# Optimization experiments

Measured on AMD Instinct MI355X. Metric: run time of the kernel, lower is better.

The kernel has to match this reference:

```python
import jax, jax.numpy as jnp
import numpy as np

N_NODES = 10000
N_EDGES = 640000
NF = 128      # n_features
NH = 128      # n_hidden
NT = 128      # n_targets
LN_EPS = 1e-5


def _layer_norm(h, gamma, beta):
    mu = jnp.mean(h, axis=-1, keepdims=True)
    var = jnp.var(h, axis=-1, keepdims=True)
    return (h - mu) * jax.lax.rsqrt(var + LN_EPS) * gamma + beta


def _mlp(h, W1, b1, gamma, beta, W2, b2):
    h = jax.nn.relu(h @ W1 + b1)
    h = _layer_norm(h, gamma, beta)
    return h @ W2 + b2


def setup_inputs() -> dict:
    key = jax.random.key(0)
    ks = jax.random.split(key, 12)
    s_in = 1.0 / np.sqrt(NF + NH)
    s_h = 1.0 / np.sqrt(NH)
    return {
        "x": jax.random.normal(ks[0], (N_NODES, NF), dtype=jnp.float32),
        "edge_idx": jax.random.randint(ks[1], (2, N_EDGES), 0, N_NODES, dtype=jnp.int32),
        "edge_attr": jax.random.normal(ks[2], (N_EDGES, NH), dtype=jnp.float32),
        # node_mlp_1 params
        "W1a": jax.random.normal(ks[3], (NF + NH, NH), dtype=jnp.float32) * s_in,
        "b1a": jnp.zeros((NH,), dtype=jnp.float32),
        "g1": jnp.ones((NH,), dtype=jnp.float32),
        "be1": jnp.zeros((NH,), dtype=jnp.float32),
        "W1b": jax.random.normal(ks[4], (NH, NH), dtype=jnp.float32) * s_h,
        "b1b": jnp.zeros((NH,), dtype=jnp.float32),
        # node_mlp_2 params
        "W2a": jax.random.normal(ks[5], (NF + NH, NH), dtype=jnp.float32) * s_in,
        "b2a": jnp.zeros((NH,), dtype=jnp.float32),
        "g2": jnp.ones((NH,), dtype=jnp.float32),
        "be2": jnp.zeros((NH,), dtype=jnp.float32),
        "W2b": jax.random.normal(ks[6], (NH, NT), dtype=jnp.float32) * s_h,
        "b2b": jnp.zeros((NT,), dtype=jnp.float32),
    }


def reference(x, edge_idx, edge_attr, W1a, b1a, g1, be1, W1b, b1b,
              W2a, b2a, g2, be2, W2b, b2b):
    row, col = edge_idx[0], edge_idx[1]
    # gather source-node features and run per-edge MLP
    h = jnp.concatenate([x[col], edge_attr], axis=1)        # [E, NF+NH]
    h = _mlp(h, W1a, b1a, g1, be1, W1b, b1b)                 # [E, NH]
    # scatter_mean into target nodes
    sums = jax.ops.segment_sum(h, row, num_segments=N_NODES)
    cnt = jax.ops.segment_sum(jnp.ones((h.shape[0],), h.dtype), row,
                              num_segments=N_NODES)
    agg = sums / jnp.maximum(cnt, 1.0)[:, None]              # [N, NH]
    out = jnp.concatenate([x, agg], axis=1)                  # [N, NF+NH]
    return _mlp(out, W2a, b2a, g2, be2, W2b, b2b)            # [N, NT]
```

## Files before the change

### kernel.cpp

```cpp
#include <hip/hip_runtime.h>
#include <hip/hip_bf16.h>

#define NN 10000
#define NE 640000
#define NF 128
#define NH 128
#define NT 128
#define KA 256
#define LN_EPS 1e-5f

typedef __bf16 bf16x8 __attribute__((ext_vector_type(8)));
typedef float floatx4 __attribute__((ext_vector_type(4)));
typedef float nfloat4 __attribute__((ext_vector_type(4)));

__device__ inline unsigned short f2bf(float f) {
    unsigned int u = __float_as_uint(f);
    u += 0x7FFFu + ((u >> 16) & 1u);
    return (unsigned short)(u >> 16);
}

__device__ inline bf16x8 load_frag(const unsigned short* p) {
    uint4 u = *(const uint4*)p;
    return __builtin_bit_cast(bf16x8, u);
}

__global__ __launch_bounds__(256) void conv_weights(
    const float* __restrict__ W1a, const float* __restrict__ W1b,
    const float* __restrict__ W2a, const float* __restrict__ W2b,
    unsigned short* __restrict__ wp1a, unsigned short* __restrict__ wp1b,
    unsigned short* __restrict__ wp2a, unsigned short* __restrict__ wp2b)
{
    int tid = blockIdx.x * 256 + threadIdx.x;
    const float* src;
    unsigned short* dst;
    int t, nks;
    if (tid < 4096)        { src = W1a; dst = wp1a; t = tid;         nks = 8; }
    else if (tid < 6144)   { src = W1b; dst = wp1b; t = tid - 4096;  nks = 4; }
    else if (tid < 10240)  { src = W2a; dst = wp2a; t = tid - 6144;  nks = 8; }
    else if (tid < 12288)  { src = W2b; dst = wp2b; t = tid - 10240; nks = 4; }
    else return;

    const int f = t >> 6, l = t & 63;
    const int ct = f / nks, ks = f - ct * nks;
    const int n  = ct * 16 + (l & 15);
    const int k0 = ks * 32 + (l >> 4) * 8;
    unsigned short tmp[8];
#pragma unroll
    for (int j = 0; j < 8; ++j)
        tmp[j] = f2bf(src[(k0 + j) * 128 + n]);
    *(uint4*)&dst[t * 8] = *(const uint4*)tmp;
}

__global__ __launch_bounds__(256) void hist_kernel(
    const int* __restrict__ row, int* __restrict__ hist)
{
    int e = blockIdx.x * 256 + threadIdx.x;
    if (e < NE) atomicAdd(&hist[row[e]], 1);
}

__global__ __launch_bounds__(256) void scan_kernel(
    const int* __restrict__ hist, int* __restrict__ row_start,
    int* __restrict__ cursor)
{
    __shared__ int partials[256];
    const int t = threadIdx.x;
    const int base = t * 40;
    int s = 0;
    for (int i = 0; i < 40; ++i) {
        int b = base + i;
        if (b < NN) s += hist[b];
    }
    partials[t] = s;
    __syncthreads();
    int pre = 0;
    for (int i = 0; i < t; ++i) pre += partials[i];
    int run = pre;
    for (int i = 0; i < 40; ++i) {
        int b = base + i;
        if (b < NN) {
            row_start[b] = run;
            cursor[b] = run;
            run += hist[b];
        }
    }
    if (t == 255) row_start[NN] = NE;
}

__global__ __launch_bounds__(256) void scatter_kernel(
    const int* __restrict__ row, int* __restrict__ cursor,
    int* __restrict__ perm)
{
    int e = blockIdx.x * 256 + threadIdx.x;
    if (e < NE) {
        int p = atomicAdd(&cursor[row[e]], 1);
        perm[p] = e;
    }
}

__global__ __launch_bounds__(256) void edge_mlp_kernel(
    const float* __restrict__ x,
    const int* __restrict__ erow, const int* __restrict__ ecol,
    const float* __restrict__ eattr,
    const int* __restrict__ perm,
    const unsigned short* __restrict__ wp1a, const float* __restrict__ b1a,
    const float* __restrict__ g1, const float* __restrict__ be1,
    const unsigned short* __restrict__ wp1b,
    float* __restrict__ sums)
{
    __shared__ float accbuf[64][132];
    __shared__ unsigned short Ttile[4][16][NH + 8];
    __shared__ int rows_s[64];
    unsigned short (*Atile)[16][KA + 8] = (unsigned short (*)[16][KA + 8])accbuf;

    const int wave = threadIdx.x >> 6;
    const int lane = threadIdx.x & 63;
    const int e0 = blockIdx.x * 64 + wave * 16;

    if (threadIdx.x < 64) {
        int e = perm[blockIdx.x * 64 + threadIdx.x];
        rows_s[threadIdx.x] = erow[e];
    }

    {
        const int lrow = lane >> 2;
        const int lq   = lane & 3;
        const int e = perm[e0 + lrow];
        const int src = ecol[e];
        const nfloat4* xr = (const nfloat4*)(x + src * NF);
        const nfloat4* ar = (const nfloat4*)(eattr + (size_t)e * NH);
        unsigned short* Ar = &Atile[wave][lrow][0];
#pragma unroll
        for (int it = 0; it < 8; ++it) {
            int c4 = lq + it * 4;
            nfloat4 v = xr[c4];
            uint2 w;
            w.x = (unsigned)f2bf(v.x) | ((unsigned)f2bf(v.y) << 16);
            w.y = (unsigned)f2bf(v.z) | ((unsigned)f2bf(v.w) << 16);
            *(uint2*)&Ar[c4 * 4] = w;
            nfloat4 v2 = __builtin_nontemporal_load(ar + c4);
            uint2 w2;
            w2.x = (unsigned)f2bf(v2.x) | ((unsigned)f2bf(v2.y) << 16);
            w2.y = (unsigned)f2bf(v2.z) | ((unsigned)f2bf(v2.w) << 16);
            *(uint2*)&Ar[128 + c4 * 4] = w2;
        }
    }
    __syncthreads();

    const int lm  = lane & 15;
    const int lq4 = lane >> 4;

    bf16x8 a1[8];
#pragma unroll
    for (int ks = 0; ks < 8; ++ks)
        a1[ks] = load_frag(&Atile[wave][lm][ks * 32 + lq4 * 8]);

    floatx4 acc1[8];
#pragma unroll
    for (int ct = 0; ct < 8; ++ct) {
        floatx4 acc = {0.f, 0.f, 0.f, 0.f};
        const unsigned short* wr = wp1a + (ct * 8 * 64 + lane) * 8;
#pragma unroll
        for (int ks = 0; ks < 8; ++ks) {
            bf16x8 b = load_frag(wr + ks * 512);
            acc = __builtin_amdgcn_mfma_f32_16x16x32_bf16(a1[ks], b, acc, 0, 0, 0);
        }
        acc1[ct] = acc;
    }

    float sum_[4] = {0, 0, 0, 0}, sq_[4] = {0, 0, 0, 0};
#pragma unroll
    for (int ct = 0; ct < 8; ++ct) {
        const float bb = b1a[ct * 16 + lm];
#pragma unroll
        for (int i = 0; i < 4; ++i) {
            float v = acc1[ct][i] + bb;
            v = fmaxf(v, 0.f);
            acc1[ct][i] = v;
            sum_[i] += v;
            sq_[i]  += v * v;
        }
    }
#pragma unroll
    for (int m = 1; m < 16; m <<= 1) {
#pragma unroll
        for (int i = 0; i < 4; ++i) {
            sum_[i] += __shfl_xor(sum_[i], m, 64);
            sq_[i]  += __shfl_xor(sq_[i],  m, 64);
        }
    }
    float mu[4], rs[4];
#pragma unroll
    for (int i = 0; i < 4; ++i) {
        mu[i] = sum_[i] * (1.f / NH);
        float var = sq_[i] * (1.f / NH) - mu[i] * mu[i];
        rs[i] = rsqrtf(var + LN_EPS);
    }
#pragma unroll
    for (int ct = 0; ct < 8; ++ct) {
        const int c = ct * 16 + lm;
        const float gg = g1[c], bb = be1[c];
#pragma unroll
        for (int i = 0; i < 4; ++i) {
            float nv = (acc1[ct][i] - mu[i]) * rs[i] * gg + bb;
            Ttile[wave][lq4 * 4 + i][c] = f2bf(nv);
        }
    }
    __syncthreads();

    bf16x8 a2[4];
#pragma unroll
    for (int ks = 0; ks < 4; ++ks)
        a2[ks] = load_frag(&Ttile[wave][lm][ks * 32 + lq4 * 8]);

#pragma unroll
    for (int ct = 0; ct < 8; ++ct) {
        floatx4 acc = {0.f, 0.f, 0.f, 0.f};
        const unsigned short* wr = wp1b + (ct * 4 * 64 + lane) * 8;
#pragma unroll
        for (int ks = 0; ks < 4; ++ks) {
            bf16x8 b = load_frag(wr + ks * 512);
            acc = __builtin_amdgcn_mfma_f32_16x16x32_bf16(a2[ks], b, acc, 0, 0, 0);
        }
        const int c = ct * 16 + lm;
#pragma unroll
        for (int i = 0; i < 4; ++i)
            accbuf[wave * 16 + lq4 * 4 + i][c] = acc[i];
    }
    __syncthreads();

    {
        const int t = threadIdx.x;
        const int c = t & 127;
        const int jb = (t >> 7) * 32;
        float a = 0.f;
        int cur = rows_s[jb];
#pragma unroll 4
        for (int j = jb; j < jb + 32; ++j) {
            a += accbuf[j][c];
            int nxt = (j + 1 < jb + 32) ? rows_s[j + 1] : -1;
            if (nxt != cur) {
                atomicAdd(&sums[cur * NH + c], a);
                a = 0.f;
                cur = nxt;
            }
        }
    }
}

__global__ __launch_bounds__(256) void node_mlp_kernel(
    const float* __restrict__ x,
    const float* __restrict__ sums, const int* __restrict__ row_start,
    const float* __restrict__ b1b,
    const unsigned short* __restrict__ wp2a, const float* __restrict__ b2a,
    const float* __restrict__ g2, const float* __restrict__ be2,
    const unsigned short* __restrict__ wp2b, const float* __restrict__ b2b,
    float* __restrict__ out)
{
    __shared__ unsigned short Atile[4][16][KA + 8];
    __shared__ unsigned short Ttile[4][16][NH + 8];

    const int wave = threadIdx.x >> 6;
    const int lane = threadIdx.x & 63;
    const int n0 = blockIdx.x * 64 + wave * 16;

    {
        const int lrow = lane >> 2;
        const int lq   = lane & 3;
        int n = n0 + lrow;
        if (n >= NN) n = NN - 1;
        const int cntn = row_start[n + 1] - row_start[n];
        const float inv  = (cntn > 0) ? (1.f / (float)cntn) : 1.f;
        const float addb = (cntn > 0) ? 1.f : 0.f;
        const float4* xr = (const float4*)(x + n * NF);
        const float4* sr = (const float4*)(sums + n * NH);
        const float4* br = (const float4*)b1b;
        unsigned short* Ar = &Atile[wave][lrow][0];
#pragma unroll
        for (int it = 0; it < 8; ++it) {
            int c4 = lq + it * 4;
            float4 v = xr[c4];
            uint2 w;
            w.x = (unsigned)f2bf(v.x) | ((unsigned)f2bf(v.y) << 16);
            w.y = (unsigned)f2bf(v.z) | ((unsigned)f2bf(v.w) << 16);
            *(uint2*)&Ar[c4 * 4] = w;
            float4 v2 = sr[c4];
            float4 bv = br[c4];
            float a0 = v2.x * inv + addb * bv.x;
            float a1 = v2.y * inv + addb * bv.y;
            float a2 = v2.z * inv + addb * bv.z;
            float a3 = v2.w * inv + addb * bv.w;
            uint2 w2;
            w2.x = (unsigned)f2bf(a0) | ((unsigned)f2bf(a1) << 16);
            w2.y = (unsigned)f2bf(a2) | ((unsigned)f2bf(a3) << 16);
            *(uint2*)&Ar[128 + c4 * 4] = w2;
        }
    }
    __syncthreads();

    const int lm  = lane & 15;
    const int lq4 = lane >> 4;

    bf16x8 a1[8];
#pragma unroll
    for (int ks = 0; ks < 8; ++ks)
        a1[ks] = load_frag(&Atile[wave][lm][ks * 32 + lq4 * 8]);

    floatx4 acc1[8];
#pragma unroll
    for (int ct = 0; ct < 8; ++ct) {
        floatx4 acc = {0.f, 0.f, 0.f, 0.f};
        const unsigned short* wr = wp2a + (ct * 8 * 64 + lane) * 8;
#pragma unroll
        for (int ks = 0; ks < 8; ++ks) {
            bf16x8 b = load_frag(wr + ks * 512);
            acc = __builtin_amdgcn_mfma_f32_16x16x32_bf16(a1[ks], b, acc, 0, 0, 0);
        }
        acc1[ct] = acc;
    }

    float sum_[4] = {0, 0, 0, 0}, sq_[4] = {0, 0, 0, 0};
#pragma unroll
    for (int ct = 0; ct < 8; ++ct) {
        const float bb = b2a[ct * 16 + lm];
#pragma unroll
        for (int i = 0; i < 4; ++i) {
            float v = acc1[ct][i] + bb;
            v = fmaxf(v, 0.f);
            acc1[ct][i] = v;
            sum_[i] += v;
            sq_[i]  += v * v;
        }
    }
#pragma unroll
    for (int m = 1; m < 16; m <<= 1) {
#pragma unroll
        for (int i = 0; i < 4; ++i) {
            sum_[i] += __shfl_xor(sum_[i], m, 64);
            sq_[i]  += __shfl_xor(sq_[i],  m, 64);
        }
    }
    float mu[4], rs[4];
#pragma unroll
    for (int i = 0; i < 4; ++i) {
        mu[i] = sum_[i] * (1.f / NH);
        float var = sq_[i] * (1.f / NH) - mu[i] * mu[i];
        rs[i] = rsqrtf(var + LN_EPS);
    }
#pragma unroll
    for (int ct = 0; ct < 8; ++ct) {
        const int c = ct * 16 + lm;
        const float gg = g2[c], bb = be2[c];
#pragma unroll
        for (int i = 0; i < 4; ++i) {
            float nv = (acc1[ct][i] - mu[i]) * rs[i] * gg + bb;
            Ttile[wave][lq4 * 4 + i][c] = f2bf(nv);
        }
    }
    __syncthreads();

    bf16x8 a2[4];
#pragma unroll
    for (int ks = 0; ks < 4; ++ks)
        a2[ks] = load_frag(&Ttile[wave][lm][ks * 32 + lq4 * 8]);

#pragma unroll
    for (int ct = 0; ct < 8; ++ct) {
        floatx4 acc = {0.f, 0.f, 0.f, 0.f};
        const unsigned short* wr = wp2b + (ct * 4 * 64 + lane) * 8;
#pragma unroll
        for (int ks = 0; ks < 4; ++ks) {
            bf16x8 b = load_frag(wr + ks * 512);
            acc = __builtin_amdgcn_mfma_f32_16x16x32_bf16(a2[ks], b, acc, 0, 0, 0);
        }
        const int c = ct * 16 + lm;
        const float bb = b2b[c];
#pragma unroll
        for (int i = 0; i < 4; ++i) {
            int n = n0 + lq4 * 4 + i;
            if (n < NN) out[n * NT + c] = acc[i] + bb;
        }
    }
}

extern "C" void kernel_launch(void* const* d_in, const int* in_sizes, int n_in,
                              void* d_out, int out_size, void* d_ws, size_t ws_size,
                              hipStream_t stream) {
    const float* x     = (const float*)d_in[0];
    const int*   eidx  = (const int*)d_in[1];
    const float* eattr = (const float*)d_in[2];
    const float* W1a = (const float*)d_in[3];
    const float* b1a = (const float*)d_in[4];
    const float* g1  = (const float*)d_in[5];
    const float* be1 = (const float*)d_in[6];
    const float* W1b = (const float*)d_in[7];
    const float* b1b = (const float*)d_in[8];
    const float* W2a = (const float*)d_in[9];
    const float* b2a = (const float*)d_in[10];
    const float* g2  = (const float*)d_in[11];
    const float* be2 = (const float*)d_in[12];
    const float* W2b = (const float*)d_in[13];
    const float* b2b = (const float*)d_in[14];

    char* ws = (char*)d_ws;
    float* sums     = (float*)ws;
    int*   hist     = (int*)(ws + 5120000);
    int*   cursor   = (int*)(ws + 5160000);
    int*   row_start= (int*)(ws + 5200000);
    int*   perm     = (int*)(ws + 5240064);
    unsigned short* wp1a = (unsigned short*)(ws + 7800064);
    unsigned short* wp1b = (unsigned short*)(ws + 7865600);
    unsigned short* wp2a = (unsigned short*)(ws + 7898368);
    unsigned short* wp2b = (unsigned short*)(ws + 7963904);

    const int* erow = eidx;
    const int* ecol = eidx + NE;

    (void)hipMemsetAsync(ws, 0, 5160000, stream);
    conv_weights<<<48, 256, 0, stream>>>(W1a, W1b, W2a, W2b, wp1a, wp1b, wp2a, wp2b);
    hist_kernel<<<(NE + 255) / 256, 256, 0, stream>>>(erow, hist);
    scan_kernel<<<1, 256, 0, stream>>>(hist, row_start, cursor);
    scatter_kernel<<<(NE + 255) / 256, 256, 0, stream>>>(erow, cursor, perm);
    edge_mlp_kernel<<<NE / 64, 256, 0, stream>>>(x, erow, ecol, eattr, perm,
                                                 wp1a, b1a, g1, be1, wp1b, sums);
    node_mlp_kernel<<<(NN + 63) / 64, 256, 0, stream>>>(x, sums, row_start, b1b,
                                                        wp2a, b2a, g2, be2, wp2b, b2b,
                                                        (float*)d_out);
}
```

Measured before the change: 716.7 us.

## Split edge MLP output columns across waves, keeping weight fragments in registers

The edge MLP kernel is restructured so each wave owns two 16-column output tiles for all 64 edges of the block, instead of all 128 columns for its own 16 edges. Each wave now loads its weight fragments once into registers, where before every wave streamed the full weight matrices from global memory. The A operand is staged in LDS in fragment-major order, and the LayerNorm statistics are combined across waves through a small shared partials buffer. The accumulation buffer uses a rotated (swizzled) layout to avoid bank conflicts, and a launch-bounds occupancy hint is added. In exchange it needs more block-wide syncs and a cross-wave LayerNorm reduction.

Result: no change. 709.8 us (-1.0%).

```diff
diff --git a/kernel.cpp b/kernel.cpp
--- a/kernel.cpp
+++ b/kernel.cpp
@@ -97,7 +97,7 @@
     }
 }
 
-__global__ __launch_bounds__(256) void edge_mlp_kernel(
+__global__ __launch_bounds__(256, 3) void edge_mlp_kernel(
     const float* __restrict__ x,
     const int* __restrict__ erow, const int* __restrict__ ecol,
     const float* __restrict__ eattr,
@@ -107,139 +107,182 @@
     const unsigned short* __restrict__ wp1b,
     float* __restrict__ sums)
 {
-    __shared__ float accbuf[64][132];
-    __shared__ unsigned short Ttile[4][16][NH + 8];
+    __shared__ __align__(16) unsigned short Afrag[16384];
+    __shared__ unsigned short Ttile[64][NH + 8];
+    __shared__ float2 partials[4][64];
+    __shared__ float2 murs[64];
     __shared__ int rows_s[64];
-    unsigned short (*Atile)[16][KA + 8] = (unsigned short (*)[16][KA + 8])accbuf;
 
     const int wave = threadIdx.x >> 6;
     const int lane = threadIdx.x & 63;
-    const int e0 = blockIdx.x * 64 + wave * 16;
+    const int lm   = lane & 15;
+    const int lq4  = lane >> 4;
+    const int e0   = blockIdx.x * 64;
+
+    if (threadIdx.x < 64)
+        rows_s[threadIdx.x] = erow[perm[e0 + threadIdx.x]];
+
+    {
+        const int r = wave * 16 + lm;
+        const int e = perm[e0 + r];
+        const int scol = ecol[e];
+        const nfloat4* xr = (const nfloat4*)(x + (size_t)scol * NF) + lq4 * 2;
+        const nfloat4* ar = (const nfloat4*)(eattr + (size_t)e * NH) + lq4 * 2;
+        unsigned short* dst = &Afrag[(wave * 8) * 512 + lane * 8];
+#pragma unroll
+        for (int ks = 0; ks < 8; ++ks) {
+            nfloat4 v0, v1;
+            if (ks < 4) {
+                v0 = xr[ks * 8];
+                v1 = xr[ks * 8 + 1];
+            } else {
+                v0 = __builtin_nontemporal_load(ar + (ks - 4) * 8);
+                v1 = __builtin_nontemporal_load(ar + (ks - 4) * 8 + 1);
+            }
+            uint4 wv;
+            wv.x = (unsigned)f2bf(v0.x) | ((unsigned)f2bf(v0.y) << 16);
+            wv.y = (unsigned)f2bf(v0.z) | ((unsigned)f2bf(v0.w) << 16);
+            wv.z = (unsigned)f2bf(v1.x) | ((unsigned)f2bf(v1.y) << 16);
+            wv.w = (unsigned)f2bf(v1.z) | ((unsigned)f2bf(v1.w) << 16);
+            *(uint4*)(dst + ks * 512) = wv;
+        }
+    }
+
+    bf16x8 b1f[2][8];
+#pragma unroll
+    for (int c = 0; c < 2; ++c) {
+        const int ct = wave * 2 + c;
+#pragma unroll
+        for (int ks = 0; ks < 8; ++ks)
+            b1f[c][ks] = load_frag(&wp1a[((ct * 8 + ks) * 64 + lane) * 8]);
+    }
+
+    __syncthreads();
+
+    floatx4 acc1[4][2];
+#pragma unroll
+    for (int mt = 0; mt < 4; ++mt) {
+        bf16x8 a[8];
+#pragma unroll
+        for (int ks = 0; ks < 8; ++ks)
+            a[ks] = load_frag(&Afrag[(mt * 8 + ks) * 512 + lane * 8]);
+#pragma unroll
+        for (int c = 0; c < 2; ++c) {
+            floatx4 acc = {0.f, 0.f, 0.f, 0.f};
+#pragma unroll
+            for (int ks = 0; ks < 8; ++ks)
+                acc = __builtin_amdgcn_mfma_f32_16x16x32_bf16(a[ks], b1f[c][ks], acc, 0, 0, 0);
+            acc1[mt][c] = acc;
+        }
+    }
+
+    const float bb0 = b1a[(wave * 2 + 0) * 16 + lm];
+    const float bb1 = b1a[(wave * 2 + 1) * 16 + lm];
+#pragma unroll
+    for (int mt = 0; mt < 4; ++mt) {
+#pragma unroll
+        for (int i = 0; i < 4; ++i) {
+            float v0 = fmaxf(acc1[mt][0][i] + bb0, 0.f);
+            float v1 = fmaxf(acc1[mt][1][i] + bb1, 0.f);
+            acc1[mt][0][i] = v0;
+            acc1[mt][1][i] = v1;
+            float s = v0 + v1;
+            float q = v0 * v0 + v1 * v1;
+#pragma unroll
+            for (int m = 1; m < 16; m <<= 1) {
+                s += __shfl_xor(s, m, 64);
+                q += __shfl_xor(q, m, 64);
+            }
+            if (lm == 0)
+                partials[wave][mt * 16 + lq4 * 4 + i] = make_float2(s, q);
+        }
+    }
+    __syncthreads();
 
     if (threadIdx.x < 64) {
-        int e = perm[blockIdx.x * 64 + threadIdx.x];
-        rows_s[threadIdx.x] = erow[e];
-    }
-
-    {
-        const int lrow = lane >> 2;
-        const int lq   = lane & 3;
-        const int e = perm[e0 + lrow];
-        const int src = ecol[e];
-        const nfloat4* xr = (const nfloat4*)(x + src * NF);
-        const nfloat4* ar = (const nfloat4*)(eattr + (size_t)e * NH);
-        unsigned short* Ar = &Atile[wave][lrow][0];
-#pragma unroll
-        for (int it = 0; it < 8; ++it) {
-            int c4 = lq + it * 4;
-            nfloat4 v = xr[c4];
-            uint2 w;
-            w.x = (unsigned)f2bf(v.x) | ((unsigned)f2bf(v.y) << 16);
-            w.y = (unsigned)f2bf(v.z) | ((unsigned)f2bf(v.w) << 16);
-            *(uint2*)&Ar[c4 * 4] = w;
-            nfloat4 v2 = __builtin_nontemporal_load(ar + c4);
-            uint2 w2;
-            w2.x = (unsigned)f2bf(v2.x) | ((unsigned)f2bf(v2.y) << 16);
-            w2.y = (unsigned)f2bf(v2.z) | ((unsigned)f2bf(v2.w) << 16);
-            *(uint2*)&Ar[128 + c4 * 4] = w2;
-        }
-    }
-    __syncthreads();
-
-    const int lm  = lane & 15;
-    const int lq4 = lane >> 4;
-
-    bf16x8 a1[8];
-#pragma unroll
-    for (int ks = 0; ks < 8; ++ks)
-        a1[ks] = load_frag(&Atile[wave][lm][ks * 32 + lq4 * 8]);
-
-    floatx4 acc1[8];
-#pragma unroll
-    for (int ct = 0; ct < 8; ++ct) {
-        floatx4 acc = {0.f, 0.f, 0.f, 0.f};
-        const unsigned short* wr = wp1a + (ct * 8 * 64 + lane) * 8;
-#pragma unroll
-        for (int ks = 0; ks < 8; ++ks) {
-            bf16x8 b = load_frag(wr + ks * 512);
-            acc = __builtin_amdgcn_mfma_f32_16x16x32_bf16(a1[ks], b, acc, 0, 0, 0);
-        }
-        acc1[ct] = acc;
-    }
-
-    float sum_[4] = {0, 0, 0, 0}, sq_[4] = {0, 0, 0, 0};
-#pragma unroll
-    for (int ct = 0; ct < 8; ++ct) {
-        const float bb = b1a[ct * 16 + lm];
-#pragma unroll
-        for (int i = 0; i < 4; ++i) {
-            float v = acc1[ct][i] + bb;
-            v = fmaxf(v, 0.f);
-            acc1[ct][i] = v;
-            sum_[i] += v;
-            sq_[i]  += v * v;
-        }
-    }
-#pragma unroll
-    for (int m = 1; m < 16; m <<= 1) {
-#pragma unroll
-        for (int i = 0; i < 4; ++i) {
-            sum_[i] += __shfl_xor(sum_[i], m, 64);
-            sq_[i]  += __shfl_xor(sq_[i],  m, 64);
-        }
-    }
-    float mu[4], rs[4];
-#pragma unroll
-    for (int i = 0; i < 4; ++i) {
-        mu[i] = sum_[i] * (1.f / NH);
-        float var = sq_[i] * (1.f / NH) - mu[i] * mu[i];
-        rs[i] = rsqrtf(var + LN_EPS);
-    }
-#pragma unroll
-    for (int ct = 0; ct < 8; ++ct) {
-        const int c = ct * 16 + lm;
-        const float gg = g1[c], bb = be1[c];
-#pragma unroll
-        for (int i = 0; i < 4; ++i) {
-            float nv = (acc1[ct][i] - mu[i]) * rs[i] * gg + bb;
-            Ttile[wave][lq4 * 4 + i][c] = f2bf(nv);
-        }
-    }
-    __syncthreads();
-
-    bf16x8 a2[4];
-#pragma unroll
-    for (int ks = 0; ks < 4; ++ks)
-        a2[ks] = load_frag(&Ttile[wave][lm][ks * 32 + lq4 * 8]);
-
-#pragma unroll
-    for (int ct = 0; ct < 8; ++ct) {
-        floatx4 acc = {0.f, 0.f, 0.f, 0.f};
-        const unsigned short* wr = wp1b + (ct * 4 * 64 + lane) * 8;
-#pragma unroll
-        for (int ks = 0; ks < 4; ++ks) {
-            bf16x8 b = load_frag(wr + ks * 512);
-            acc = __builtin_amdgcn_mfma_f32_16x16x32_bf16(a2[ks], b, acc, 0, 0, 0);
-        }
-        const int c = ct * 16 + lm;
-#pragma unroll
-        for (int i = 0; i < 4; ++i)
-            accbuf[wave * 16 + lq4 * 4 + i][c] = acc[i];
+        float s = 0.f, q = 0.f;
+#pragma unroll
+        for (int w2 = 0; w2 < 4; ++w2) {
+            float2 p = partials[w2][threadIdx.x];
+            s += p.x; q += p.y;
+        }
+        float mu = s * (1.f / NH);
+        float var = q * (1.f / NH) - mu * mu;
+        murs[threadIdx.x] = make_float2(mu, rsqrtf(var + LN_EPS));
+    }
+    __syncthreads();
+
+    bf16x8 b2f[2][4];
+#pragma unroll
+    for (int c = 0; c < 2; ++c) {
+        const int ct = wave * 2 + c;
+#pragma unroll
+        for (int ks = 0; ks < 4; ++ks)
+            b2f[c][ks] = load_frag(&wp1b[((ct * 4 + ks) * 64 + lane) * 8]);
+    }
+
+    const float gg0 = g1[(wave * 2 + 0) * 16 + lm];
+    const float ee0 = be1[(wave * 2 + 0) * 16 + lm];
+    const float gg1 = g1[(wave * 2 + 1) * 16 + lm];
+    const float ee1 = be1[(wave * 2 + 1) * 16 + lm];
+#pragma unroll
+    for (int mt = 0; mt < 4; ++mt) {
+#pragma unroll
+        for (int i = 0; i < 4; ++i) {
+            const int row = mt * 16 + lq4 * 4 + i;
+            float2 mr = murs[row];
+            float n0 = (acc1[mt][0][i] - mr.x) * mr.y * gg0 + ee0;
+            float n1 = (acc1[mt][1][i] - mr.x) * mr.y * gg1 + ee1;
+            Ttile[row][(wave * 2 + 0) * 16 + lm] = f2bf(n0);
+            Ttile[row][(wave * 2 + 1) * 16 + lm] = f2bf(n1);
+        }
+    }
+    __syncthreads();
+
+    floatx4 acc2[4][2];
+#pragma unroll
+    for (int mt = 0; mt < 4; ++mt) {
+        bf16x8 a[4];
+#pragma unroll
+        for (int ks = 0; ks < 4; ++ks)
+            a[ks] = load_frag(&Ttile[mt * 16 + lm][ks * 32 + lq4 * 8]);
+#pragma unroll
+        for (int c = 0; c < 2; ++c) {
+            floatx4 acc = {0.f, 0.f, 0.f, 0.f};
+#pragma unroll
+            for (int ks = 0; ks < 4; ++ks)
+                acc = __builtin_amdgcn_mfma_f32_16x16x32_bf16(a[ks], b2f[c][ks], acc, 0, 0, 0);
+            acc2[mt][c] = acc;
+        }
+    }
+
+    float* accbuf = (float*)Afrag;
+#pragma unroll
+    for (int mt = 0; mt < 4; ++mt) {
+#pragma unroll
+        for (int c = 0; c < 2; ++c) {
+            const int col = (wave * 2 + c) * 16 + lm;
+#pragma unroll
+            for (int i = 0; i < 4; ++i) {
+                const int row = mt * 16 + lq4 * 4 + i;
+                accbuf[row * 128 + ((col + row * 4) & 127)] = acc2[mt][c][i];
+            }
+        }
     }
     __syncthreads();
 
     {
         const int t = threadIdx.x;
-        const int c = t & 127;
+        const int cc = t & 127;
         const int jb = (t >> 7) * 32;
         float a = 0.f;
         int cur = rows_s[jb];
 #pragma unroll 4
         for (int j = jb; j < jb + 32; ++j) {
-            a += accbuf[j][c];
+            a += accbuf[j * 128 + ((cc + j * 4) & 127)];
             int nxt = (j + 1 < jb + 32) ? rows_s[j + 1] : -1;
             if (nxt != cur) {
-                atomicAdd(&sums[cur * NH + c], a);
+                atomicAdd(&sums[cur * NH + cc], a);
                 a = 0.f;
                 cur = nxt;
             }
```

## Load edge MLP A-fragments directly from global and slim shared memory

Applied to the files above, without the earlier changes.

The edge MLP kernel now loads each lane's x and edge_attr slices straight into the MFMA A-fragment registers, converting them with native bf16 casts. This removes the shared-memory staging tile and its block barrier. The LayerNorm output tile is aliased into each wave's private slice of the accumulation buffer, with only a compiler memory fence instead of __syncthreads. The accumulation buffer is unpadded and column-swizzled to avoid bank conflicts, and launch bounds request 4 blocks per CU. The per-lane global loads are less coalesced than the old cooperative row loads, and forcing occupancy could increase register pressure.

After: 773.9 us. +8.0%, slower.

```diff
diff --git a/kernel.cpp b/kernel.cpp
--- a/kernel.cpp
+++ b/kernel.cpp
@@ -22,6 +22,13 @@
 __device__ inline bf16x8 load_frag(const unsigned short* p) {
     uint4 u = *(const uint4*)p;
     return __builtin_bit_cast(bf16x8, u);
+}
+
+__device__ inline bf16x8 cvt8(nfloat4 v0, nfloat4 v1) {
+    bf16x8 r;
+    r[0] = (__bf16)v0.x; r[1] = (__bf16)v0.y; r[2] = (__bf16)v0.z; r[3] = (__bf16)v0.w;
+    r[4] = (__bf16)v1.x; r[5] = (__bf16)v1.y; r[6] = (__bf16)v1.z; r[7] = (__bf16)v1.w;
+    return r;
 }
 
 __global__ __launch_bounds__(256) void conv_weights(
@@ -97,7 +104,7 @@
     }
 }
 
-__global__ __launch_bounds__(256) void edge_mlp_kernel(
+__global__ __launch_bounds__(256, 4) void edge_mlp_kernel(
     const float* __restrict__ x,
     const int* __restrict__ erow, const int* __restrict__ ecol,
     const float* __restrict__ eattr,
@@ -107,52 +114,36 @@
     const unsigned short* __restrict__ wp1b,
     float* __restrict__ sums)
 {
-    __shared__ float accbuf[64][132];
-    __shared__ unsigned short Ttile[4][16][NH + 8];
+    __shared__ __align__(16) float accbuf[64 * 128];
     __shared__ int rows_s[64];
-    unsigned short (*Atile)[16][KA + 8] = (unsigned short (*)[16][KA + 8])accbuf;
 
     const int wave = threadIdx.x >> 6;
     const int lane = threadIdx.x & 63;
-    const int e0 = blockIdx.x * 64 + wave * 16;
-
-    if (threadIdx.x < 64) {
-        int e = perm[blockIdx.x * 64 + threadIdx.x];
-        rows_s[threadIdx.x] = erow[e];
-    }
-
-    {
-        const int lrow = lane >> 2;
-        const int lq   = lane & 3;
-        const int e = perm[e0 + lrow];
-        const int src = ecol[e];
-        const nfloat4* xr = (const nfloat4*)(x + src * NF);
-        const nfloat4* ar = (const nfloat4*)(eattr + (size_t)e * NH);
-        unsigned short* Ar = &Atile[wave][lrow][0];
-#pragma unroll
-        for (int it = 0; it < 8; ++it) {
-            int c4 = lq + it * 4;
-            nfloat4 v = xr[c4];
-            uint2 w;
-            w.x = (unsigned)f2bf(v.x) | ((unsigned)f2bf(v.y) << 16);
-            w.y = (unsigned)f2bf(v.z) | ((unsigned)f2bf(v.w) << 16);
-            *(uint2*)&Ar[c4 * 4] = w;
-            nfloat4 v2 = __builtin_nontemporal_load(ar + c4);
-            uint2 w2;
-            w2.x = (unsigned)f2bf(v2.x) | ((unsigned)f2bf(v2.y) << 16);
-            w2.y = (unsigned)f2bf(v2.z) | ((unsigned)f2bf(v2.w) << 16);
-            *(uint2*)&Ar[128 + c4 * 4] = w2;
-        }
-    }
-    __syncthreads();
-
-    const int lm  = lane & 15;
-    const int lq4 = lane >> 4;
+    const int lm   = lane & 15;
+    const int lq4  = lane >> 4;
+    const int e0   = blockIdx.x * 64;
+
+    if (threadIdx.x < 64)
+        rows_s[threadIdx.x] = erow[perm[e0 + threadIdx.x]];
+
+    const int e    = perm[e0 + wave * 16 + lm];
+    const int scol = ecol[e];
+    const nfloat4* xr = (const nfloat4*)(x + (size_t)scol * NF) + lq4 * 2;
+    const nfloat4* ar = (const nfloat4*)(eattr + (size_t)e * NH) + lq4 * 2;
 
     bf16x8 a1[8];
 #pragma unroll
-    for (int ks = 0; ks < 8; ++ks)
-        a1[ks] = load_frag(&Atile[wave][lm][ks * 32 + lq4 * 8]);
+    for (int ks = 0; ks < 4; ++ks) {
+        nfloat4 v0 = xr[ks * 8];
+        nfloat4 v1 = xr[ks * 8 + 1];
+        a1[ks] = cvt8(v0, v1);
+    }
+#pragma unroll
+    for (int ks = 0; ks < 4; ++ks) {
+        nfloat4 v0 = __builtin_nontemporal_load(ar + ks * 8);
+        nfloat4 v1 = __builtin_nontemporal_load(ar + ks * 8 + 1);
+        a1[4 + ks] = cvt8(v0, v1);
+    }
 
     floatx4 acc1[8];
 #pragma unroll
@@ -195,6 +186,8 @@
         float var = sq_[i] * (1.f / NH) - mu[i] * mu[i];
         rs[i] = rsqrtf(var + LN_EPS);
     }
+
+    unsigned short* Tw = (unsigned short*)(accbuf + wave * 16 * 128);
 #pragma unroll
     for (int ct = 0; ct < 8; ++ct) {
         const int c = ct * 16 + lm;
@@ -202,15 +195,15 @@
 #pragma unroll
         for (int i = 0; i < 4; ++i) {
             float nv = (acc1[ct][i] - mu[i]) * rs[i] * gg + bb;
-            Ttile[wave][lq4 * 4 + i][c] = f2bf(nv);
-        }
-    }
-    __syncthreads();
+            Tw[(lq4 * 4 + i) * 136 + c] = __builtin_bit_cast(unsigned short, (__bf16)nv);
+        }
+    }
+    asm volatile("" ::: "memory");
 
     bf16x8 a2[4];
 #pragma unroll
     for (int ks = 0; ks < 4; ++ks)
-        a2[ks] = load_frag(&Ttile[wave][lm][ks * 32 + lq4 * 8]);
+        a2[ks] = load_frag(&Tw[lm * 136 + ks * 32 + lq4 * 8]);
 
 #pragma unroll
     for (int ct = 0; ct < 8; ++ct) {
@@ -223,23 +216,25 @@
         }
         const int c = ct * 16 + lm;
 #pragma unroll
-        for (int i = 0; i < 4; ++i)
-            accbuf[wave * 16 + lq4 * 4 + i][c] = acc[i];
+        for (int i = 0; i < 4; ++i) {
+            const int r = wave * 16 + lq4 * 4 + i;
+            accbuf[r * 128 + ((c + r * 4) & 127)] = acc[i];
+        }
     }
     __syncthreads();
 
     {
         const int t = threadIdx.x;
-        const int c = t & 127;
+        const int cc = t & 127;
         const int jb = (t >> 7) * 32;
         float a = 0.f;
         int cur = rows_s[jb];
 #pragma unroll 4
         for (int j = jb; j < jb + 32; ++j) {
-            a += accbuf[j][c];
+            a += accbuf[j * 128 + ((cc + j * 4) & 127)];
             int nxt = (j + 1 < jb + 32) ? rows_s[j + 1] : -1;
             if (nxt != cur) {
-                atomicAdd(&sums[cur * NH + c], a);
+                atomicAdd(&sums[cur * NH + cc], a);
                 a = 0.f;
                 cur = nxt;
             }
```

## Fuse whole GNN pipeline into one persistent cooperative kernel with grid syncs

Applied to the files above, without the earlier changes.

Replaces the memset plus six separate launches with a single cooperative persistent kernel that runs zeroing, weight conversion, histogram, scan, scatter, edge MLP and node MLP as phases separated by grid-wide syncs. It also pre-converts x to bf16 once so edge gathers read half the bytes, and assigns edge tiles to blocks grouped by XCD for locality. This targets launch overheads and gaps between small kernels, at the cost of a serial single-block scan phase, grid-sync costs and a capped occupancy of 3 blocks per CU. It falls back to the old multi-kernel path if cooperative launch is unavailable.

Measured after the change: 1.999 ms. +178.9%, slower.

```diff
diff --git a/kernel.cpp b/kernel.cpp
--- a/kernel.cpp
+++ b/kernel.cpp
@@ -1,5 +1,8 @@
 #include <hip/hip_runtime.h>
 #include <hip/hip_bf16.h>
+#include <hip/hip_cooperative_groups.h>
+
+namespace cg = cooperative_groups;
 
 #define NN 10000
 #define NE 640000
@@ -8,6 +11,7 @@
 #define NT 128
 #define KA 256
 #define LN_EPS 1e-5f
+#define NNT 157
 
 typedef __bf16 bf16x8 __attribute__((ext_vector_type(8)));
 typedef float floatx4 __attribute__((ext_vector_type(4)));
@@ -22,6 +26,380 @@
 __device__ inline bf16x8 load_frag(const unsigned short* p) {
     uint4 u = *(const uint4*)p;
     return __builtin_bit_cast(bf16x8, u);
+}
+
+__device__ inline bf16x8 cvt8(nfloat4 v0, nfloat4 v1) {
+    bf16x8 r;
+    r[0] = (__bf16)v0.x; r[1] = (__bf16)v0.y; r[2] = (__bf16)v0.z; r[3] = (__bf16)v0.w;
+    r[4] = (__bf16)v1.x; r[5] = (__bf16)v1.y; r[6] = (__bf16)v1.z; r[7] = (__bf16)v1.w;
+    return r;
+}
+
+__device__ inline void lds_fence() {
+    asm volatile("s_waitcnt lgkmcnt(0)" ::: "memory");
+}
+
+__global__ __launch_bounds__(256, 3) void fused_kernel(
+    const float* __restrict__ x,
+    const int* __restrict__ eidx,
+    const float* __restrict__ eattr,
+    const float* __restrict__ W1a, const float* __restrict__ b1a,
+    const float* __restrict__ g1,  const float* __restrict__ be1,
+    const float* __restrict__ W1b, const float* __restrict__ b1b,
+    const float* __restrict__ W2a, const float* __restrict__ b2a,
+    const float* __restrict__ g2,  const float* __restrict__ be2,
+    const float* __restrict__ W2b, const float* __restrict__ b2b,
+    float* __restrict__ sums, int* __restrict__ hist, int* __restrict__ cursor,
+    int* __restrict__ row_start, int* __restrict__ perm,
+    unsigned short* __restrict__ wp1a, unsigned short* __restrict__ wp1b,
+    unsigned short* __restrict__ wp2a, unsigned short* __restrict__ wp2b,
+    unsigned short* __restrict__ xbf,
+    float* __restrict__ out)
+{
+    cg::grid_group gridg = cg::this_grid();
+    __shared__ __align__(16) float smem[12864];
+
+    const int nb  = gridDim.x;
+    const int nth = nb * 256;
+    const int tid = blockIdx.x * 256 + threadIdx.x;
+    const int* erow = eidx;
+    const int* ecol = eidx + NE;
+
+    const int wave = threadIdx.x >> 6;
+    const int lane = threadIdx.x & 63;
+    const int lm   = lane & 15;
+    const int lq4  = lane >> 4;
+
+    {
+        uint4 z = {0u, 0u, 0u, 0u};
+        uint4* zp = (uint4*)sums;
+        for (int i = tid; i < 322500; i += nth) zp[i] = z;
+
+        const nfloat4* xs = (const nfloat4*)x;
+        uint4* xd = (uint4*)xbf;
+        for (int i = tid; i < 160000; i += nth)
+            xd[i] = __builtin_bit_cast(uint4, cvt8(xs[i * 2], xs[i * 2 + 1]));
+
+        if (tid < 12288) {
+            const float* src; unsigned short* dst; int t, nks;
+            if (tid < 4096)       { src = W1a; dst = wp1a; t = tid;         nks = 8; }
+            else if (tid < 6144)  { src = W1b; dst = wp1b; t = tid - 4096;  nks = 4; }
+            else if (tid < 10240) { src = W2a; dst = wp2a; t = tid - 6144;  nks = 8; }
+            else                  { src = W2b; dst = wp2b; t = tid - 10240; nks = 4; }
+            const int f = t >> 6, l = t & 63;
+            const int ct = f / nks, ks = f - ct * nks;
+            const int n  = ct * 16 + (l & 15);
+            const int k0 = ks * 32 + (l >> 4) * 8;
+            unsigned short tmp[8];
+#pragma unroll
+            for (int j = 0; j < 8; ++j)
+                tmp[j] = f2bf(src[(k0 + j) * 128 + n]);
+            *(uint4*)&dst[t * 8] = *(const uint4*)tmp;
+        }
+    }
+    __threadfence();
+    gridg.sync();
+
+    for (int e = tid; e < NE; e += nth)
+        atomicAdd(&hist[erow[e]], 1);
+    __threadfence();
+    gridg.sync();
+
+    if (blockIdx.x == 0) {
+        int* partials = (int*)smem;
+        const int t = threadIdx.x;
+        const int base = t * 40;
+        int s = 0;
+        for (int i = 0; i < 40; ++i) {
+            int b = base + i;
+            if (b < NN) s += hist[b];
+        }
+        partials[t] = s;
+        __syncthreads();
+        int pre = 0;
+        for (int i = 0; i < t; ++i) pre += partials[i];
+        int run = pre;
+        for (int i = 0; i < 40; ++i) {
+            int b = base + i;
+            if (b < NN) {
+                row_start[b] = run;
+                cursor[b] = run;
+                run += hist[b];
+            }
+        }
+        if (t == 255) row_start[NN] = NE;
+    }
+    __threadfence();
+    gridg.sync();
+
+    for (int e = tid; e < NE; e += nth) {
+        int p = atomicAdd(&cursor[erow[e]], 1);
+        perm[p] = e;
+    }
+    __threadfence();
+    gridg.sync();
+
+    {
+        float* accbuf = smem;
+        unsigned short (*Atile)[KA + 8] =
+            (unsigned short (*)[KA + 8])smem;
+        unsigned short* Tt = (unsigned short*)smem + 16896;
+        int* rows_s = (int*)((char*)smem + 51200);
+
+        const int xcd = blockIdx.x & 7;
+        const int lx  = blockIdx.x >> 3;
+        const int pxb = nb >> 3;
+        const int t1  = xcd * 1250 + 1250;
+
+        for (int tile = xcd * 1250 + lx; tile < t1; tile += pxb) {
+            const int e0 = tile * 64;
+            if (threadIdx.x < 64)
+                rows_s[threadIdx.x] = erow[perm[e0 + threadIdx.x]];
+
+            {
+                const int lrow = lane >> 2;
+                const int lq   = lane & 3;
+                const int e = perm[e0 + wave * 16 + lrow];
+                const int scol = ecol[e];
+                const uint4* xr = (const uint4*)(xbf + (size_t)scol * NF);
+                const nfloat4* ar = (const nfloat4*)(eattr + (size_t)e * NH);
+                unsigned short* Ar = &Atile[wave * 16 + lrow][0];
+#pragma unroll
+                for (int it = 0; it < 4; ++it) {
+                    const int g = lq + it * 4;
+                    *(uint4*)&Ar[g * 8] = xr[g];
+                }
+#pragma unroll
+                for (int it = 0; it < 4; ++it) {
+                    const int g = lq + it * 4;
+                    nfloat4 v0 = __builtin_nontemporal_load(ar + g * 2);
+                    nfloat4 v1 = __builtin_nontemporal_load(ar + g * 2 + 1);
+                    *(uint4*)&Ar[128 + g * 8] = __builtin_bit_cast(uint4, cvt8(v0, v1));
+                }
+            }
+            lds_fence();
+
+            bf16x8 a1[8];
+#pragma unroll
+            for (int ks = 0; ks < 8; ++ks)
+                a1[ks] = load_frag(&Atile[wave * 16 + lm][ks * 32 + lq4 * 8]);
+
+            floatx4 acc1[8];
+#pragma unroll
+            for (int ct = 0; ct < 8; ++ct) {
+                floatx4 acc = {0.f, 0.f, 0.f, 0.f};
+                const unsigned short* wr = wp1a + (ct * 8 * 64 + lane) * 8;
+#pragma unroll
+                for (int ks = 0; ks < 8; ++ks) {
+                    bf16x8 b = load_frag(wr + ks * 512);
+                    acc = __builtin_amdgcn_mfma_f32_16x16x32_bf16(a1[ks], b, acc, 0, 0, 0);
+                }
+                acc1[ct] = acc;
+            }
+
+            float sum_[4] = {0, 0, 0, 0}, sq_[4] = {0, 0, 0, 0};
+#pragma unroll
+            for (int ct = 0; ct < 8; ++ct) {
+                const float bb = b1a[ct * 16 + lm];
+#pragma unroll
+                for (int i = 0; i < 4; ++i) {
+                    float v = acc1[ct][i] + bb;
+                    v = fmaxf(v, 0.f);
+                    acc1[ct][i] = v;
+                    sum_[i] += v;
+                    sq_[i]  += v * v;
+                }
+            }
+#pragma unroll
+            for (int m = 1; m < 16; m <<= 1) {
+#pragma unroll
+                for (int i = 0; i < 4; ++i) {
+                    sum_[i] += __shfl_xor(sum_[i], m, 64);
+                    sq_[i]  += __shfl_xor(sq_[i],  m, 64);
+                }
+            }
+            float mu[4], rs[4];
+#pragma unroll
+            for (int i = 0; i < 4; ++i) {
+                mu[i] = sum_[i] * (1.f / NH);
+                float var = sq_[i] * (1.f / NH) - mu[i] * mu[i];
+                rs[i] = rsqrtf(var + LN_EPS);
+            }
+
+#pragma unroll
+            for (int ct = 0; ct < 8; ++ct) {
+                const int c = ct * 16 + lm;
+                const float gg = g1[c], bb = be1[c];
+#pragma unroll
+                for (int i = 0; i < 4; ++i) {
+                    float nv = (acc1[ct][i] - mu[i]) * rs[i] * gg + bb;
+                    Tt[(wave * 16 + lq4 * 4 + i) * 136 + c] = f2bf(nv);
+                }
+            }
+            lds_fence();
+
+            bf16x8 a2[4];
+#pragma unroll
+            for (int ks = 0; ks < 4; ++ks)
+                a2[ks] = load_frag(&Tt[(wave * 16 + lm) * 136 + ks * 32 + lq4 * 8]);
+
+#pragma unroll
+            for (int ct = 0; ct < 8; ++ct) {
+                floatx4 acc = {0.f, 0.f, 0.f, 0.f};
+                const unsigned short* wr = wp1b + (ct * 4 * 64 + lane) * 8;
+#pragma unroll
+                for (int ks = 0; ks < 4; ++ks) {
+                    bf16x8 b = load_frag(wr + ks * 512);
+                    acc = __builtin_amdgcn_mfma_f32_16x16x32_bf16(a2[ks], b, acc, 0, 0, 0);
+                }
+                const int c = ct * 16 + lm;
+#pragma unroll
+                for (int i = 0; i < 4; ++i)
+                    accbuf[(wave * 16 + lq4 * 4 + i) * 132 + c] = acc[i];
+            }
+            __syncthreads();
+
+            {
+                const int t = threadIdx.x;
+                const int cc = t & 127;
+                const int jb = (t >> 7) * 32;
+                float a = 0.f;
+                int cur = rows_s[jb];
+#pragma unroll 4
+                for (int j = jb; j < jb + 32; ++j) {
+                    a += accbuf[j * 132 + cc];
+                    int nxt = (j + 1 < jb + 32) ? rows_s[j + 1] : -1;
+                    if (nxt != cur) {
+                        atomicAdd(&sums[cur * NH + cc], a);
+                        a = 0.f;
+                        cur = nxt;
+                    }
+                }
+            }
+            __syncthreads();
+        }
+    }
+    __threadfence();
+    gridg.sync();
+
+    if (blockIdx.x < NNT) {
+        unsigned short (*Atile)[KA + 8] = (unsigned short (*)[KA + 8])smem;
+        unsigned short* Tt = (unsigned short*)smem + 16896;
+        const int n0 = blockIdx.x * 64 + wave * 16;
+
+        {
+            const int lrow = lane >> 2;
+            const int lq   = lane & 3;
+            int n = n0 + lrow;
+            if (n >= NN) n = NN - 1;
+            const int cntn = row_start[n + 1] - row_start[n];
+            const float inv  = (cntn > 0) ? (1.f / (float)cntn) : 1.f;
+            const float addb = (cntn > 0) ? 1.f : 0.f;
+            const uint4* xr = (const uint4*)(xbf + (size_t)n * NF);
+            const nfloat4* sr = (const nfloat4*)(sums + (size_t)n * NH);
+            const nfloat4* br = (const nfloat4*)b1b;
+            unsigned short* Ar = &Atile[wave * 16 + lrow][0];
+#pragma unroll
+            for (int it = 0; it < 4; ++it) {
+                const int g = lq + it * 4;
+                *(uint4*)&Ar[g * 8] = xr[g];
+            }
+#pragma unroll
+            for (int it = 0; it < 4; ++it) {
+                const int g = lq + it * 4;
+                nfloat4 s0 = sr[g * 2], s1 = sr[g * 2 + 1];
+                nfloat4 c0 = br[g * 2], c1 = br[g * 2 + 1];
+                nfloat4 u0, u1;
+                u0.x = s0.x * inv + addb * c0.x;  u0.y = s0.y * inv + addb * c0.y;
+                u0.z = s0.z * inv + addb * c0.z;  u0.w = s0.w * inv + addb * c0.w;
+                u1.x = s1.x * inv + addb * c1.x;  u1.y = s1.y * inv + addb * c1.y;
+                u1.z = s1.z * inv + addb * c1.z;  u1.w = s1.w * inv + addb * c1.w;
+                *(uint4*)&Ar[128 + g * 8] = __builtin_bit_cast(uint4, cvt8(u0, u1));
+            }
+        }
+        __syncthreads();
+
+        bf16x8 a1[8];
+#pragma unroll
+        for (int ks = 0; ks < 8; ++ks)
+            a1[ks] = load_frag(&Atile[wave * 16 + lm][ks * 32 + lq4 * 8]);
+
+        floatx4 acc1[8];
+#pragma unroll
+        for (int ct = 0; ct < 8; ++ct) {
+            floatx4 acc = {0.f, 0.f, 0.f, 0.f};
+            const unsigned short* wr = wp2a + (ct * 8 * 64 + lane) * 8;
+#pragma unroll
+            for (int ks = 0; ks < 8; ++ks) {
+                bf16x8 b = load_frag(wr + ks * 512);
+                acc = __builtin_amdgcn_mfma_f32_16x16x32_bf16(a1[ks], b, acc, 0, 0, 0);
+            }
+            acc1[ct] = acc;
+        }
+
+        float sum_[4] = {0, 0, 0, 0}, sq_[4] = {0, 0, 0, 0};
+#pragma unroll
+        for (int ct = 0; ct < 8; ++ct) {
+            const float bb = b2a[ct * 16 + lm];
+#pragma unroll
+            for (int i = 0; i < 4; ++i) {
+                float v = acc1[ct][i] + bb;
+                v = fmaxf(v, 0.f);
+                acc1[ct][i] = v;
+                sum_[i] += v;
+                sq_[i]  += v * v;
+            }
+        }
+#pragma unroll
+        for (int m = 1; m < 16; m <<= 1) {
+#pragma unroll
+            for (int i = 0; i < 4; ++i) {
+                sum_[i] += __shfl_xor(sum_[i], m, 64);
+                sq_[i]  += __shfl_xor(sq_[i],  m, 64);
+            }
+        }
+        float mu[4], rs[4];
+#pragma unroll
+        for (int i = 0; i < 4; ++i) {
+            mu[i] = sum_[i] * (1.f / NH);
+            float var = sq_[i] * (1.f / NH) - mu[i] * mu[i];
+            rs[i] = rsqrtf(var + LN_EPS);
+        }
+#pragma unroll
+        for (int ct = 0; ct < 8; ++ct) {
+            const int c = ct * 16 + lm;
+            const float gg = g2[c], bb = be2[c];
+#pragma unroll
+            for (int i = 0; i < 4; ++i) {
+                float nv = (acc1[ct][i] - mu[i]) * rs[i] * gg + bb;
+                Tt[(wave * 16 + lq4 * 4 + i) * 136 + c] = f2bf(nv);
+            }
+        }
+        __syncthreads();
+
+        bf16x8 a2[4];
+#pragma unroll
+        for (int ks = 0; ks < 4; ++ks)
+            a2[ks] = load_frag(&Tt[(wave * 16 + lm) * 136 + ks * 32 + lq4 * 8]);
+
+#pragma unroll
+        for (int ct = 0; ct < 8; ++ct) {
+            floatx4 acc = {0.f, 0.f, 0.f, 0.f};
+            const unsigned short* wr = wp2b + (ct * 4 * 64 + lane) * 8;
+#pragma unroll
+            for (int ks = 0; ks < 4; ++ks) {
+                bf16x8 b = load_frag(wr + ks * 512);
+                acc = __builtin_amdgcn_mfma_f32_16x16x32_bf16(a2[ks], b, acc, 0, 0, 0);
+            }
+            const int c = ct * 16 + lm;
+            const float bb = b2b[c];
+#pragma unroll
+            for (int i = 0; i < 4; ++i) {
+                int n = n0 + lq4 * 4 + i;
+                if (n < NN) out[n * NT + c] = acc[i] + bb;
+            }
+        }
+    }
 }
 
 __global__ __launch_bounds__(256) void conv_weights(
@@ -402,18 +780,56 @@
     const float* b2b = (const float*)d_in[14];
 
     char* ws = (char*)d_ws;
-    float* sums     = (float*)ws;
-    int*   hist     = (int*)(ws + 5120000);
-    int*   cursor   = (int*)(ws + 5160000);
-    int*   row_start= (int*)(ws + 5200000);
-    int*   perm     = (int*)(ws + 5240064);
+    float* sums      = (float*)ws;
+    int*   hist      = (int*)(ws + 5120000);
+    int*   cursor    = (int*)(ws + 5160000);
+    int*   row_start = (int*)(ws + 5200000);
+    int*   perm      = (int*)(ws + 5240064);
     unsigned short* wp1a = (unsigned short*)(ws + 7800064);
     unsigned short* wp1b = (unsigned short*)(ws + 7865600);
     unsigned short* wp2a = (unsigned short*)(ws + 7898368);
     unsigned short* wp2b = (unsigned short*)(ws + 7963904);
+    unsigned short* xbf  = (unsigned short*)(ws + 7996672);
+    float* out = (float*)d_out;
 
     const int* erow = eidx;
     const int* ecol = eidx + NE;
+
+    static int nblocks = 0;
+    if (nblocks == 0) {
+        int dev = 0;
+        (void)hipGetDevice(&dev);
+        int coop = 0;
+        (void)hipDeviceGetAttribute(&coop, hipDeviceAttributeCooperativeLaunch, dev);
+        int maxb = 0;
+        if (coop && ws_size >= 10556672) {
+            if (hipOccupancyMaxActiveBlocksPerMultiprocessor(&maxb, fused_kernel, 256, 0)
+                != hipSuccess) maxb = 0;
+        }
+        if (maxb >= 3)      nblocks = 768;
+        else if (maxb == 2) nblocks = 512;
+        else if (maxb == 1) nblocks = 256;
+        else                nblocks = -1;
+    }
+
+    if (nblocks > 0) {
+        void* args[] = {
+            (void*)&x, (void*)&eidx, (void*)&eattr,
+            (void*)&W1a, (void*)&b1a, (void*)&g1, (void*)&be1,
+            (void*)&W1b, (void*)&b1b,
+            (void*)&W2a, (void*)&b2a, (void*)&g2, (void*)&be2,
+            (void*)&W2b, (void*)&b2b,
+            (void*)&sums, (void*)&hist, (void*)&cursor,
+            (void*)&row_start, (void*)&perm,
+            (void*)&wp1a, (void*)&wp1b, (void*)&wp2a, (void*)&wp2b,
+            (void*)&xbf, (void*)&out
+        };
+        hipError_t err = hipLaunchCooperativeKernel((void*)fused_kernel,
+                                                    dim3(nblocks), dim3(256),
+                                                    args, 0, stream);
+        if (err == hipSuccess) return;
+        nblocks = -1;
+    }
 
     (void)hipMemsetAsync(ws, 0, 5160000, stream);
     conv_weights<<<48, 256, 0, stream>>>(W1a, W1b, W2a, W2b, wp1a, wp1b, wp2a, wp2b);
@@ -424,5 +840,5 @@
                                                  wp1a, b1a, g1, be1, wp1b, sums);
     node_mlp_kernel<<<(NN + 63) / 64, 256, 0, stream>>>(x, sums, row_start, b1b,
                                                         wp2a, b2a, g2, be2, wp2b, b2b,
-                                                        (float*)d_out);
-}
+                                                        out);
+}
```
